# Kernel tuning notes

Hardware: AMD Instinct MI355X
Metric: run time of the kernel (lower is better)

## Reference

```python
import jax, jax.numpy as jnp
import numpy as np

B, S, E = 2, 2048, 1024
N_HEADS = 16
HEAD_DIM = E // N_HEADS  # 64
ATTN_SCALE = 1.0 / np.sqrt(E)  # NOTE: original scales by 1/sqrt(hidden_dim_phi), not head_dim
ROPE_BASE = 10000.0


def _rope(t):
    # t: (B, H, S, D) with D = HEAD_DIM; interleaved-pair RoPE (torchtune-style)
    d = t.shape[-1]
    s = t.shape[-2]
    inv_freq = 1.0 / (ROPE_BASE ** (jnp.arange(0, d, 2, dtype=jnp.float32) / d))  # (D/2,)
    ang = jnp.arange(s, dtype=jnp.float32)[:, None] * inv_freq[None, :]  # (S, D/2)
    cos, sin = jnp.cos(ang), jnp.sin(ang)  # (S, D/2)
    tp = t.reshape(t.shape[:-1] + (d // 2, 2))
    te, to = tp[..., 0], tp[..., 1]  # (B,H,S,D/2)
    oe = te * cos - to * sin
    oo = te * sin + to * cos
    return jnp.stack([oe, oo], axis=-1).reshape(t.shape)


def setup_inputs() -> dict:
    key = jax.random.key(0)
    ks = jax.random.split(key, 5)
    std = 0.02
    return {
        "x": jax.random.normal(ks[0], (B, S, E), dtype=jnp.float32),
        "W_q": jax.random.normal(ks[1], (E, E), dtype=jnp.float32) * std,
        "W_k": jax.random.normal(ks[2], (E, E), dtype=jnp.float32) * std,
        "W_v": jax.random.normal(ks[3], (E, E), dtype=jnp.float32) * std,
        "W_o": jax.random.normal(ks[4], (E, E), dtype=jnp.float32) * std,
    }


def reference(x, W_q, W_k, W_v, W_o):
    b, s, e = x.shape
    hd = e // N_HEADS
    # projections -> (B, H, S, D)
    def proj(w):
        return (x @ w).reshape(b, s, N_HEADS, hd).transpose(0, 2, 1, 3)
    q = _rope(proj(W_q))
    k = _rope(proj(W_k))
    v = proj(W_v)
    scores = jnp.einsum('bhsd,bhtd->bhst', q, k) * ATTN_SCALE  # (B,H,S,S)
    causal = jnp.triu(jnp.ones((s, s), dtype=bool), k=1)
    scores = jnp.where(causal, -jnp.inf, scores)
    probs = jax.nn.softmax(scores, axis=-1)  # dropout is identity in eval mode
    out = jnp.einsum('bhst,bhtd->bhsd', probs, v)
    out = out.transpose(0, 2, 1, 3).reshape(b, s, e)
    return out @ W_o
```

## Files before the change

kernel.cpp:

```cpp
#include <hip/hip_runtime.h>
#include <hip/hip_bf16.h>

#define S_LEN 2048
#define E_DIM 1024
#define NH 16
#define HD 64
#define ATTN_SCALE 0.03125f
#define QSCALE_L2E 0.045084312f
#define KVB 128

typedef __attribute__((ext_vector_type(8))) short short8;
typedef __attribute__((ext_vector_type(8))) unsigned short ushort8;
typedef __attribute__((ext_vector_type(4))) unsigned short ushort4_t;
typedef __attribute__((ext_vector_type(4))) float f32x4;
typedef __attribute__((ext_vector_type(4))) float f4;
typedef __attribute__((ext_vector_type(2))) unsigned int uint2_t;

__device__ __forceinline__ float bf2f(unsigned short u) {
    unsigned int x = ((unsigned int)u) << 16;
    return __builtin_bit_cast(float, x);
}
__device__ __forceinline__ unsigned short f2bf(float f) {
    unsigned int x = __builtin_bit_cast(unsigned int, f);
    x += 0x7FFFu + ((x >> 16) & 1u);
    return (unsigned short)(x >> 16);
}
__device__ __forceinline__ float exp2_fast(float x) {
    float r;
    asm("v_exp_f32 %0, %1" : "=v"(r) : "v"(x));
    return r;
}
__device__ __forceinline__ void gload16(const unsigned short* g, unsigned short* l) {
    __builtin_amdgcn_global_load_lds(
        (__attribute__((address_space(1))) void*)g,
        (__attribute__((address_space(3))) void*)l, 16, 0, 0);
}

__global__ __launch_bounds__(256) void k_prep(const float* __restrict__ x,
                                              unsigned short* __restrict__ xb,
                                              const float* W0, const float* W1,
                                              const float* W2, const float* W3,
                                              unsigned short* Tqkv,
                                              unsigned short* Twout,
                                              float* __restrict__ cosT,
                                              float* __restrict__ sinT) {
    int bid = blockIdx.x;
    int tid = threadIdx.x;
    if (bid < 2048) {
        size_t i = ((size_t)bid * 256 + tid) * 8;
        f4 a = *(const f4*)(x + i);
        f4 b = *(const f4*)(x + i + 4);
        ushort8 o;
        o[0] = f2bf(a[0]); o[1] = f2bf(a[1]); o[2] = f2bf(a[2]); o[3] = f2bf(a[3]);
        o[4] = f2bf(b[0]); o[5] = f2bf(b[1]); o[6] = f2bf(b[2]); o[7] = f2bf(b[3]);
        *(ushort8*)(xb + i) = o;
    } else if (bid < 2304) {
        int idx = (bid - 2048) * 256 + tid;
        int s = idx >> 5, j = idx & 31;
        float inv = expf(-(float)j * (9.210340371976184f / 32.f));
        float ang = (float)s * inv;
        cosT[idx] = cosf(ang);
        sinT[idx] = sinf(ang);
    } else {
        int t = bid - 2304;
        int bx = (t & 31) * 32, by = ((t >> 5) & 31) * 32, z = t >> 10;
        const float* W; unsigned short* T;
        switch (z) {
            case 0: W = W0; T = Tqkv; break;
            case 1: W = W1; T = Tqkv + 1048576; break;
            case 2: W = W2; T = Tqkv + 2097152; break;
            default: W = W3; T = Twout; break;
        }
        __shared__ float tile[32][33];
        int tx = tid & 31, ty = tid >> 5;
#pragma unroll
        for (int i = 0; i < 4; i++)
            tile[ty + i * 8][tx] = W[(size_t)(by + ty + i * 8) * E_DIM + bx + tx];
        __syncthreads();
#pragma unroll
        for (int i = 0; i < 4; i++)
            T[(size_t)(bx + ty + i * 8) * E_DIM + by + tx] = f2bf(tile[tx][ty + i * 8]);
    }
}

__global__ __launch_bounds__(256, 3)
void k_gemm97(const unsigned short* __restrict__ A,
              const unsigned short* __restrict__ B,
              unsigned short* __restrict__ Qo,
              unsigned short* __restrict__ Ko,
              unsigned short* __restrict__ Vto,
              const float* __restrict__ cosT,
              const float* __restrict__ sinT) {
    constexpr int NBN = 24;
    constexpr int NWG = 32 * NBN;
    __shared__ unsigned short Alds[128 * 64];
    __shared__ unsigned short Blds[128 * 64];
    int tid = threadIdx.x, lane = tid & 63, wid = tid >> 6;
    int l15 = lane & 15, lg = lane >> 4;
    int wr = wid >> 1, wc = wid & 1;
    int orig = blockIdx.y * NBN + blockIdx.x;
    int wg = (orig & 7) * (NWG / 8) + (orig >> 3);
    int bm = wg / NBN, bn = wg % NBN;

    f32x4 acc[4][4] = {};
    for (int k0 = 0; k0 < E_DIM; k0 += 64) {
#pragma unroll
        for (int i = 0; i < 4; i++) {
            int r = wid * 32 + i * 8 + (lane >> 3);
            int cs = (lane & 7) ^ (r & 7);
            gload16(A + (size_t)(bm * 128 + r) * E_DIM + k0 + cs * 8,
                    Alds + (wid * 256 + i * 64) * 8);
        }
#pragma unroll
        for (int i = 0; i < 4; i++) {
            int r = wid * 32 + i * 8 + (lane >> 3);
            int cs = (lane & 7) ^ (r & 7);
            gload16(B + (size_t)(bn * 128 + r) * E_DIM + k0 + cs * 8,
                    Blds + (wid * 256 + i * 64) * 8);
        }
        __syncthreads();
#pragma unroll
        for (int ks = 0; ks < 2; ks++) {
            short8 af[4], bfr[4];
#pragma unroll
            for (int mf = 0; mf < 4; mf++) {
                int r = wr * 64 + mf * 16 + l15;
                int gc = ks * 4 + lg;
                af[mf] = *(const short8*)(Alds + r * 64 + ((gc ^ (r & 7)) << 3));
            }
#pragma unroll
            for (int nf = 0; nf < 4; nf++) {
                int r = wc * 64 + nf * 16 + l15;
                int gc = ks * 4 + lg;
                bfr[nf] = *(const short8*)(Blds + r * 64 + ((gc ^ (r & 7)) << 3));
            }
            __builtin_amdgcn_s_setprio(1);
#pragma unroll
            for (int mf = 0; mf < 4; mf++)
#pragma unroll
                for (int nf = 0; nf < 4; nf++)
                    acc[mf][nf] = __builtin_amdgcn_mfma_f32_16x16x32_bf16(
                        af[mf], bfr[nf], acc[mf][nf], 0, 0, 0);
            __builtin_amdgcn_s_setprio(0);
        }
        __syncthreads();
    }
#pragma unroll
    for (int mf = 0; mf < 4; mf++) {
        int r0 = bm * 128 + wr * 64 + mf * 16 + lg * 4;
#pragma unroll
        for (int nf = 0; nf < 4; nf++) {
            int colg = bn * 128 + wc * 64 + nf * 16 + l15;
            int z = colg >> 10, c1 = colg & 1023;
            if (z == 2) {
                int h = c1 >> 6, d = c1 & 63;
                int bb = r0 >> 11, s = r0 & 2047;
                ushort4_t p;
#pragma unroll
                for (int r = 0; r < 4; r++) p[r] = f2bf(acc[mf][nf][r]);
                *(ushort4_t*)(Vto + (((size_t)((bb * 16 + h) * 64 + d)) << 11) + s) = p;
            } else {
                unsigned short* T = z ? Ko : Qo;
                int dl = c1 & 63, j = dl >> 1;
                float sgn = (dl & 1) ? 1.f : -1.f;
                float scq = z ? 1.f : QSCALE_L2E;
#pragma unroll
                for (int r = 0; r < 4; r++) {
                    int row = r0 + r, s = row & 2047;
                    float c = cosT[s * 32 + j], sn = sinT[s * 32 + j];
                    float v = acc[mf][nf][r];
                    float p = __shfl_xor(v, 1);
                    T[(size_t)row * E_DIM + c1] = f2bf((v * c + sgn * p * sn) * scq);
                }
            }
        }
    }
}

__global__ __launch_bounds__(256, 3)
void k_gemmo97(const unsigned short* __restrict__ A,
               const unsigned short* __restrict__ B,
               float* __restrict__ Fo) {
    constexpr int NBN = 16;
    constexpr int NWG = 32 * NBN;
    __shared__ unsigned short Alds[128 * 64];
    __shared__ unsigned short Blds[64 * 64];
    int tid = threadIdx.x, lane = tid & 63, wid = tid >> 6;
    int l15 = lane & 15, lg = lane >> 4;
    int wr = wid >> 1, wc = wid & 1;
    int orig = blockIdx.y * NBN + blockIdx.x;
    int wg = (orig & 7) * (NWG / 8) + (orig >> 3);
    int bm = wg / NBN, bn = wg % NBN;

    f32x4 acc[4][2] = {};
    for (int k0 = 0; k0 < E_DIM; k0 += 64) {
#pragma unroll
        for (int i = 0; i < 4; i++) {
            int r = wid * 32 + i * 8 + (lane >> 3);
            int cs = (lane & 7) ^ (r & 7);
            gload16(A + (size_t)(bm * 128 + r) * E_DIM + k0 + cs * 8,
                    Alds + (wid * 256 + i * 64) * 8);
        }
        {
#pragma unroll
            for (int i = 0; i < 2; i++) {
                int r = wid * 16 + i * 8 + (lane >> 3);
                int cs = (lane & 7) ^ (r & 7);
                gload16(B + (size_t)(bn * 64 + r) * E_DIM + k0 + cs * 8,
                        Blds + (wid * 128 + i * 64) * 8);
            }
        }
        __syncthreads();
#pragma unroll
        for (int ks = 0; ks < 2; ks++) {
            short8 af[4], bfr[2];
#pragma unroll
            for (int mf = 0; mf < 4; mf++) {
                int r = wr * 64 + mf * 16 + l15;
                int gc = ks * 4 + lg;
                af[mf] = *(const short8*)(Alds + r * 64 + ((gc ^ (r & 7)) << 3));
            }
#pragma unroll
            for (int nf = 0; nf < 2; nf++) {
                int r = wc * 32 + nf * 16 + l15;
                int gc = ks * 4 + lg;
                bfr[nf] = *(const short8*)(Blds + r * 64 + ((gc ^ (r & 7)) << 3));
            }
            __builtin_amdgcn_s_setprio(1);
#pragma unroll
            for (int mf = 0; mf < 4; mf++)
#pragma unroll
                for (int nf = 0; nf < 2; nf++)
                    acc[mf][nf] = __builtin_amdgcn_mfma_f32_16x16x32_bf16(
                        af[mf], bfr[nf], acc[mf][nf], 0, 0, 0);
            __builtin_amdgcn_s_setprio(0);
        }
        __syncthreads();
    }
#pragma unroll
    for (int mf = 0; mf < 4; mf++) {
        int r0 = bm * 128 + wr * 64 + mf * 16 + lg * 4;
#pragma unroll
        for (int nf = 0; nf < 2; nf++) {
            int colg = bn * 64 + wc * 32 + nf * 16 + l15;
#pragma unroll
            for (int r = 0; r < 4; r++)
                Fo[(size_t)(r0 + r) * E_DIM + colg] = acc[mf][nf][r];
        }
    }
}

__global__ __launch_bounds__(256, 3) void k_attn(const unsigned short* __restrict__ Q,
                                                 const unsigned short* __restrict__ K,
                                                 const unsigned short* __restrict__ Vt,
                                                 unsigned short* __restrict__ O) {
    __shared__ unsigned short K_lds[128 * 64];
    __shared__ unsigned short V_lds[64 * 128];
    __shared__ unsigned short P_lds[4][16][136];
    int tid = threadIdx.x, lane = tid & 63, wid = tid >> 6;
    int l15 = lane & 15, lg = lane >> 4;
    int orig = blockIdx.y * 32 + blockIdx.x;
    int xcd = orig & 7, idx = orig >> 3;
    int bh = xcd * 4 + (idx & 3);
    int qt = 31 - ((idx >> 2) & 31);
    int b = bh >> 4, h = bh & 15;
    const size_t base_qk = (size_t)b * S_LEN * E_DIM + (size_t)h * HD;
    const unsigned short* Vbh = Vt + ((size_t)(bh * 64) << 11);

    auto stageK = [&](int kt) {
        const unsigned short* Kb = K + base_qk + (size_t)(kt * KVB) * E_DIM;
#pragma unroll
        for (int i = 0; i < 4; i++) {
            int r = i * 32 + wid * 8 + (lane >> 3);
            int cs = (lane & 7) ^ (r & 7);
            gload16(Kb + (size_t)r * E_DIM + cs * 8, K_lds + i * 2048 + wid * 512);
        }
    };
    auto stageV = [&](int kt) {
#pragma unroll
        for (int i = 0; i < 4; i++) {
            int r = i * 16 + wid * 4 + (lane >> 4);
            int cs = (lane & 15) ^ (r & 7);
            gload16(Vbh + (size_t)r * 2048 + kt * KVB + cs * 8,
                    V_lds + i * 2048 + wid * 512);
        }
    };

    const unsigned short* Qb = Q + base_qk + (size_t)(qt * 64 + wid * 16) * E_DIM;
    short8 bq[2];
#pragma unroll
    for (int s2 = 0; s2 < 2; s2++)
        bq[s2] = *(const short8*)(Qb + (size_t)l15 * E_DIM + s2 * 32 + lg * 8);
    f32x4 acc_o[4] = {};
    float m_i = -1e30f, l_i = 0.f;
    int q_glob = qt * 64 + wid * 16 + l15;
    int nkt = (qt + 2) >> 1;
    stageK(0);
    stageV(0);
    asm volatile("s_waitcnt vmcnt(4)" ::: "memory");
    __builtin_amdgcn_s_barrier();
    __builtin_amdgcn_sched_barrier(0);
    for (int kt = 0; kt < nkt; ++kt) {
        f32x4 acc_s[8] = {};
        __builtin_amdgcn_s_setprio(1);
#pragma unroll
        for (int mf = 0; mf < 8; mf++) {
            int rK = mf * 16 + l15;
#pragma unroll
            for (int s2 = 0; s2 < 2; s2++) {
                int gc = s2 * 4 + lg;
                short8 a = *(const short8*)&K_lds[rK * 64 + ((gc ^ (rK & 7)) << 3)];
                acc_s[mf] = __builtin_amdgcn_mfma_f32_16x16x32_bf16(
                    a, bq[s2], acc_s[mf], 0, 0, 0);
            }
        }
        __builtin_amdgcn_s_setprio(0);
        __builtin_amdgcn_s_barrier();
        if (kt + 1 < nkt) stageK(kt + 1);
        float sv[32];
        float vmax = -1e30f;
        if (kt == nkt - 1) {
#pragma unroll
            for (int mf = 0; mf < 8; mf++)
#pragma unroll
                for (int r = 0; r < 4; r++) {
                    int kg = kt * KVB + mf * 16 + lg * 4 + r;
                    float v = acc_s[mf][r];
                    if (kg > q_glob) v = -1e30f;
                    sv[mf * 4 + r] = v;
                    vmax = fmaxf(vmax, v);
                }
        } else {
#pragma unroll
            for (int mf = 0; mf < 8; mf++)
#pragma unroll
                for (int r = 0; r < 4; r++) {
                    float v = acc_s[mf][r];
                    sv[mf * 4 + r] = v;
                    vmax = fmaxf(vmax, v);
                }
        }
        vmax = fmaxf(vmax, __shfl_xor(vmax, 16));
        vmax = fmaxf(vmax, __shfl_xor(vmax, 32));
        if (!__all(vmax - m_i <= 8.0f)) {
            float m_new = fmaxf(m_i, vmax);
            float corr = exp2_fast(m_i - m_new);
            l_i *= corr;
#pragma unroll
            for (int r = 0; r < 4; r++) {
                float c4 = __shfl(corr, lg * 4 + r);
#pragma unroll
                for (int nf = 0; nf < 4; nf++) acc_o[nf][r] *= c4;
            }
            m_i = m_new;
        }
        float rowsum = 0.f;
#pragma unroll
        for (int i = 0; i < 32; i++) {
            float p = exp2_fast(sv[i] - m_i);
            sv[i] = p;
            rowsum += p;
        }
        rowsum += __shfl_xor(rowsum, 16);
        rowsum += __shfl_xor(rowsum, 32);
        l_i += rowsum;
#pragma unroll
        for (int mf = 0; mf < 8; mf++) {
            unsigned int w0, w1;
            asm("v_cvt_pk_bf16_f32 %0, %1, %2"
                : "=v"(w0) : "v"(sv[mf * 4 + 0]), "v"(sv[mf * 4 + 1]));
            asm("v_cvt_pk_bf16_f32 %0, %1, %2"
                : "=v"(w1) : "v"(sv[mf * 4 + 2]), "v"(sv[mf * 4 + 3]));
            uint2_t w; w[0] = w0; w[1] = w1;
            *(uint2_t*)&P_lds[wid][l15][mf * 16 + lg * 4] = w;
        }
        if (kt + 1 < nkt)
            asm volatile("s_waitcnt vmcnt(4)" ::: "memory");
        else
            asm volatile("s_waitcnt vmcnt(0)" ::: "memory");
        __builtin_amdgcn_s_barrier();
        __builtin_amdgcn_sched_barrier(0);
        __builtin_amdgcn_s_setprio(1);
#pragma unroll
        for (int s2 = 0; s2 < 4; s2++) {
            short8 pa = *(const short8*)&P_lds[wid][l15][s2 * 32 + lg * 8];
#pragma unroll
            for (int nf = 0; nf < 4; nf++) {
                int rV = nf * 16 + l15;
                int gc = s2 * 4 + lg;
                short8 bv = *(const short8*)&V_lds[rV * 128 + ((gc ^ (rV & 7)) << 3)];
                acc_o[nf] = __builtin_amdgcn_mfma_f32_16x16x32_bf16(
                    pa, bv, acc_o[nf], 0, 0, 0);
            }
        }
        __builtin_amdgcn_s_setprio(0);
        __builtin_amdgcn_s_barrier();
        if (kt + 1 < nkt) {
            stageV(kt + 1);
            asm volatile("s_waitcnt vmcnt(4)" ::: "memory");
        }
        __builtin_amdgcn_s_barrier();
        __builtin_amdgcn_sched_barrier(0);
    }
    unsigned short* Ob = O + base_qk + (size_t)(qt * 64 + wid * 16) * E_DIM;
#pragma unroll
    for (int r = 0; r < 4; r++) {
        float linv = 1.f / __shfl(l_i, lg * 4 + r);
#pragma unroll
        for (int nf = 0; nf < 4; nf++)
            Ob[(size_t)(lg * 4 + r) * E_DIM + nf * 16 + l15] =
                f2bf(acc_o[nf][r] * linv);
    }
}

extern "C" void kernel_launch(void* const* d_in, const int* in_sizes, int n_in,
                              void* d_out, int out_size, void* d_ws, size_t ws_size,
                              hipStream_t stream) {
    (void)in_sizes; (void)n_in; (void)out_size; (void)ws_size;
    const float* x  = (const float*)d_in[0];
    const float* Wq = (const float*)d_in[1];
    const float* Wk = (const float*)d_in[2];
    const float* Wv = (const float*)d_in[3];
    const float* Wo = (const float*)d_in[4];

    unsigned short* us = (unsigned short*)d_ws;
    unsigned short* xb    = us;
    unsigned short* WqkvT = us + 4194304;
    unsigned short* WoT   = us + 7340032;
    unsigned short* Qb    = us + 8388608;
    unsigned short* Kb    = us + 12582912;
    unsigned short* Vt    = us + 16777216;
    unsigned short* AO    = us + 20971520;
    float* cosT = (float*)((char*)d_ws + 50331648);
    float* sinT = cosT + 65536;

    k_prep<<<6400, 256, 0, stream>>>(x, xb, Wq, Wk, Wv, Wo, WqkvT, WoT, cosT, sinT);
    k_gemm97<<<dim3(24, 32), 256, 0, stream>>>(xb, WqkvT, Qb, Kb, Vt, cosT, sinT);
    k_attn<<<dim3(32, 32), 256, 0, stream>>>(Qb, Kb, Vt, AO);
    k_gemmo97<<<dim3(16, 32), 256, 0, stream>>>(AO, WoT, (float*)d_out);
}
```

Baseline: 95.88 us.

## Rewrite attention with 32x32x16 MFMA, two waves per block, register-resident P

The attention kernel moves from 16x16x32 MFMAs with four waves of 16 query rows to 32x32x16 MFMAs with two waves of 32 query rows. The softmax probabilities now stay in registers, with a lane shuffle standing in for the P round trip through LDS. The lazy-rescale threshold is dropped in favour of an unconditional online-softmax correction. Output goes through an LDS staging buffer so each lane writes 16-byte vectors. This aims to cut LDS traffic and instruction count, but halving the threads per block means each wave issues twice as many K/V staging loads and there are fewer waves to hide latency.

```diff
diff --git a/kernel.cpp b/kernel.cpp
--- a/kernel.cpp
+++ b/kernel.cpp
@@ -13,8 +13,9 @@
 typedef __attribute__((ext_vector_type(8))) unsigned short ushort8;
 typedef __attribute__((ext_vector_type(4))) unsigned short ushort4_t;
 typedef __attribute__((ext_vector_type(4))) float f32x4;
+typedef __attribute__((ext_vector_type(16))) float f32x16;
 typedef __attribute__((ext_vector_type(4))) float f4;
-typedef __attribute__((ext_vector_type(2))) unsigned int uint2_t;
+typedef __attribute__((ext_vector_type(4))) unsigned int uint4v;
 
 __device__ __forceinline__ float bf2f(unsigned short u) {
     unsigned int x = ((unsigned int)u) << 16;
@@ -250,15 +251,15 @@
     }
 }
 
-__global__ __launch_bounds__(256, 3) void k_attn(const unsigned short* __restrict__ Q,
-                                                 const unsigned short* __restrict__ K,
-                                                 const unsigned short* __restrict__ Vt,
-                                                 unsigned short* __restrict__ O) {
+__global__ __launch_bounds__(128, 3)
+void k_attn(const unsigned short* __restrict__ Q,
+            const unsigned short* __restrict__ K,
+            const unsigned short* __restrict__ Vt,
+            unsigned short* __restrict__ O) {
     __shared__ unsigned short K_lds[128 * 64];
     __shared__ unsigned short V_lds[64 * 128];
-    __shared__ unsigned short P_lds[4][16][136];
     int tid = threadIdx.x, lane = tid & 63, wid = tid >> 6;
-    int l15 = lane & 15, lg = lane >> 4;
+    int l31 = lane & 31, hi = lane >> 5;
     int orig = blockIdx.y * 32 + blockIdx.x;
     int xcd = orig & 7, idx = orig >> 3;
     int bh = xcd * 4 + (idx & 3);
@@ -267,149 +268,166 @@
     const size_t base_qk = (size_t)b * S_LEN * E_DIM + (size_t)h * HD;
     const unsigned short* Vbh = Vt + ((size_t)(bh * 64) << 11);
 
+    int qbase = qt * 64 + wid * 32;
+    int q_glob = qbase + l31;
+    int nkt = (qt + 2) >> 1;
+    int swz = l31 & 7;
+    bool ishi = hi != 0;
+
     auto stageK = [&](int kt) {
         const unsigned short* Kb = K + base_qk + (size_t)(kt * KVB) * E_DIM;
 #pragma unroll
-        for (int i = 0; i < 4; i++) {
-            int r = i * 32 + wid * 8 + (lane >> 3);
+        for (int i = 0; i < 8; i++) {
+            int r = i * 16 + wid * 8 + (lane >> 3);
             int cs = (lane & 7) ^ (r & 7);
-            gload16(Kb + (size_t)r * E_DIM + cs * 8, K_lds + i * 2048 + wid * 512);
+            gload16(Kb + (size_t)r * E_DIM + cs * 8,
+                    K_lds + i * 1024 + wid * 512 + 0);
         }
     };
     auto stageV = [&](int kt) {
 #pragma unroll
-        for (int i = 0; i < 4; i++) {
-            int r = i * 16 + wid * 4 + (lane >> 4);
-            int cs = (lane & 15) ^ (r & 7);
+        for (int i = 0; i < 8; i++) {
+            int r = i * 8 + wid * 4 + (lane >> 4);
+            int c = lane & 15;
+            int cs = c ^ (r & 7);
             gload16(Vbh + (size_t)r * 2048 + kt * KVB + cs * 8,
-                    V_lds + i * 2048 + wid * 512);
+                    V_lds + i * 1024 + wid * 512);
         }
     };
 
-    const unsigned short* Qb = Q + base_qk + (size_t)(qt * 64 + wid * 16) * E_DIM;
-    short8 bq[2];
-#pragma unroll
-    for (int s2 = 0; s2 < 2; s2++)
-        bq[s2] = *(const short8*)(Qb + (size_t)l15 * E_DIM + s2 * 32 + lg * 8);
-    f32x4 acc_o[4] = {};
+    const unsigned short* Qb = Q + base_qk + (size_t)(wid * 32 + l31) * E_DIM
+                                 - (size_t)(wid * 32 + l31) * E_DIM
+                                 + (size_t)q_glob * E_DIM;
+    short8 qf[4];
+#pragma unroll
+    for (int s = 0; s < 4; s++)
+        qf[s] = *(const short8*)(Qb + s * 16 + hi * 8);
+
+    f32x16 ot0 = {}, ot1 = {};
     float m_i = -1e30f, l_i = 0.f;
-    int q_glob = qt * 64 + wid * 16 + l15;
-    int nkt = (qt + 2) >> 1;
+
     stageK(0);
     stageV(0);
-    asm volatile("s_waitcnt vmcnt(4)" ::: "memory");
+    asm volatile("s_waitcnt vmcnt(8)" ::: "memory");
     __builtin_amdgcn_s_barrier();
     __builtin_amdgcn_sched_barrier(0);
     for (int kt = 0; kt < nkt; ++kt) {
-        f32x4 acc_s[8] = {};
+        f32x16 st[4] = {};
         __builtin_amdgcn_s_setprio(1);
 #pragma unroll
-        for (int mf = 0; mf < 8; mf++) {
-            int rK = mf * 16 + l15;
-#pragma unroll
-            for (int s2 = 0; s2 < 2; s2++) {
-                int gc = s2 * 4 + lg;
-                short8 a = *(const short8*)&K_lds[rK * 64 + ((gc ^ (rK & 7)) << 3)];
-                acc_s[mf] = __builtin_amdgcn_mfma_f32_16x16x32_bf16(
-                    a, bq[s2], acc_s[mf], 0, 0, 0);
+        for (int g = 0; g < 4; g++) {
+            int row = g * 32 + l31;
+#pragma unroll
+            for (int s = 0; s < 4; s++) {
+                short8 ka = *(const short8*)
+                    &K_lds[row * 64 + (((s * 2 + hi) ^ swz) << 3)];
+                st[g] = __builtin_amdgcn_mfma_f32_32x32x16_bf16(ka, qf[s], st[g], 0, 0, 0);
             }
         }
         __builtin_amdgcn_s_setprio(0);
         __builtin_amdgcn_s_barrier();
         if (kt + 1 < nkt) stageK(kt + 1);
-        float sv[32];
         float vmax = -1e30f;
-        if (kt == nkt - 1) {
-#pragma unroll
-            for (int mf = 0; mf < 8; mf++)
-#pragma unroll
-                for (int r = 0; r < 4; r++) {
-                    int kg = kt * KVB + mf * 16 + lg * 4 + r;
-                    float v = acc_s[mf][r];
-                    if (kg > q_glob) v = -1e30f;
-                    sv[mf * 4 + r] = v;
+        bool domask = (kt * KVB + 127) > qbase;
+        if (domask) {
+#pragma unroll
+            for (int g = 0; g < 4; g++)
+#pragma unroll
+                for (int r = 0; r < 16; r++) {
+                    int kg = kt * KVB + g * 32 + (r & 3) + 8 * (r >> 2) + 4 * hi;
+                    float v = (kg > q_glob) ? -1e30f : st[g][r];
+                    st[g][r] = v;
                     vmax = fmaxf(vmax, v);
                 }
         } else {
 #pragma unroll
-            for (int mf = 0; mf < 8; mf++)
-#pragma unroll
-                for (int r = 0; r < 4; r++) {
-                    float v = acc_s[mf][r];
-                    sv[mf * 4 + r] = v;
-                    vmax = fmaxf(vmax, v);
-                }
-        }
-        vmax = fmaxf(vmax, __shfl_xor(vmax, 16));
+            for (int g = 0; g < 4; g++)
+#pragma unroll
+                for (int r = 0; r < 16; r++)
+                    vmax = fmaxf(vmax, st[g][r]);
+        }
         vmax = fmaxf(vmax, __shfl_xor(vmax, 32));
-        if (!__all(vmax - m_i <= 8.0f)) {
-            float m_new = fmaxf(m_i, vmax);
-            float corr = exp2_fast(m_i - m_new);
-            l_i *= corr;
-#pragma unroll
-            for (int r = 0; r < 4; r++) {
-                float c4 = __shfl(corr, lg * 4 + r);
-#pragma unroll
-                for (int nf = 0; nf < 4; nf++) acc_o[nf][r] *= c4;
-            }
-            m_i = m_new;
-        }
-        float rowsum = 0.f;
-#pragma unroll
-        for (int i = 0; i < 32; i++) {
-            float p = exp2_fast(sv[i] - m_i);
-            sv[i] = p;
-            rowsum += p;
-        }
-        rowsum += __shfl_xor(rowsum, 16);
-        rowsum += __shfl_xor(rowsum, 32);
-        l_i += rowsum;
-#pragma unroll
-        for (int mf = 0; mf < 8; mf++) {
-            unsigned int w0, w1;
-            asm("v_cvt_pk_bf16_f32 %0, %1, %2"
-                : "=v"(w0) : "v"(sv[mf * 4 + 0]), "v"(sv[mf * 4 + 1]));
-            asm("v_cvt_pk_bf16_f32 %0, %1, %2"
-                : "=v"(w1) : "v"(sv[mf * 4 + 2]), "v"(sv[mf * 4 + 3]));
-            uint2_t w; w[0] = w0; w[1] = w1;
-            *(uint2_t*)&P_lds[wid][l15][mf * 16 + lg * 4] = w;
-        }
+        float m_new = fmaxf(m_i, vmax);
+        float corr = exp2_fast(m_i - m_new);
+        float rs = 0.f;
+#pragma unroll
+        for (int g = 0; g < 4; g++)
+#pragma unroll
+            for (int r = 0; r < 16; r++) {
+                float p = exp2_fast(st[g][r] - m_new);
+                st[g][r] = p;
+                rs += p;
+            }
+        rs += __shfl_xor(rs, 32);
+        l_i = l_i * corr + rs;
+        m_i = m_new;
+        unsigned int pk[4][8];
+#pragma unroll
+        for (int g = 0; g < 4; g++)
+#pragma unroll
+            for (int i = 0; i < 8; i++)
+                asm("v_cvt_pk_bf16_f32 %0, %1, %2"
+                    : "=v"(pk[g][i]) : "v"(st[g][2 * i]), "v"(st[g][2 * i + 1]));
         if (kt + 1 < nkt)
-            asm volatile("s_waitcnt vmcnt(4)" ::: "memory");
+            asm volatile("s_waitcnt vmcnt(8)" ::: "memory");
         else
             asm volatile("s_waitcnt vmcnt(0)" ::: "memory");
         __builtin_amdgcn_s_barrier();
         __builtin_amdgcn_sched_barrier(0);
+#pragma unroll
+        for (int r = 0; r < 16; r++) { ot0[r] *= corr; ot1[r] *= corr; }
         __builtin_amdgcn_s_setprio(1);
 #pragma unroll
-        for (int s2 = 0; s2 < 4; s2++) {
-            short8 pa = *(const short8*)&P_lds[wid][l15][s2 * 32 + lg * 8];
-#pragma unroll
-            for (int nf = 0; nf < 4; nf++) {
-                int rV = nf * 16 + l15;
-                int gc = s2 * 4 + lg;
-                short8 bv = *(const short8*)&V_lds[rV * 128 + ((gc ^ (rV & 7)) << 3)];
-                acc_o[nf] = __builtin_amdgcn_mfma_f32_16x16x32_bf16(
-                    pa, bv, acc_o[nf], 0, 0, 0);
-            }
-        }
+        for (int g = 0; g < 4; g++)
+#pragma unroll
+            for (int ks = 0; ks < 2; ks++) {
+                int off = ks * 4;
+                unsigned int a  = pk[g][off + 0], b2 = pk[g][off + 1];
+                unsigned int c2 = pk[g][off + 2], d2 = pk[g][off + 3];
+                unsigned int sa = __shfl_xor(a, 32),  sb = __shfl_xor(b2, 32);
+                unsigned int sc = __shfl_xor(c2, 32), sd = __shfl_xor(d2, 32);
+                uint4v w;
+                w[0] = ishi ? sc : a;  w[1] = ishi ? sd : b2;
+                w[2] = ishi ? c2 : sa; w[3] = ishi ? d2 : sb;
+                short8 pf = __builtin_bit_cast(short8, w);
+                int gc = g * 4 + ks * 2 + hi;
+                short8 va0 = *(const short8*)
+                    &V_lds[l31 * 128 + ((gc ^ swz) << 3)];
+                short8 va1 = *(const short8*)
+                    &V_lds[(32 + l31) * 128 + ((gc ^ swz) << 3)];
+                ot0 = __builtin_amdgcn_mfma_f32_32x32x16_bf16(va0, pf, ot0, 0, 0, 0);
+                ot1 = __builtin_amdgcn_mfma_f32_32x32x16_bf16(va1, pf, ot1, 0, 0, 0);
+            }
         __builtin_amdgcn_s_setprio(0);
         __builtin_amdgcn_s_barrier();
         if (kt + 1 < nkt) {
             stageV(kt + 1);
-            asm volatile("s_waitcnt vmcnt(4)" ::: "memory");
-        }
-        __builtin_amdgcn_s_barrier();
-        __builtin_amdgcn_sched_barrier(0);
-    }
-    unsigned short* Ob = O + base_qk + (size_t)(qt * 64 + wid * 16) * E_DIM;
-#pragma unroll
-    for (int r = 0; r < 4; r++) {
-        float linv = 1.f / __shfl(l_i, lg * 4 + r);
-#pragma unroll
-        for (int nf = 0; nf < 4; nf++)
-            Ob[(size_t)(lg * 4 + r) * E_DIM + nf * 16 + l15] =
-                f2bf(acc_o[nf][r] * linv);
+            asm volatile("s_waitcnt vmcnt(8)" ::: "memory");
+            __builtin_amdgcn_s_barrier();
+            __builtin_amdgcn_sched_barrier(0);
+        }
+    }
+    float linv = 1.f / l_i;
+    unsigned short* scb = K_lds + wid * 2304;
+#pragma unroll
+    for (int i = 0; i < 8; i++) {
+        int d = 2 * (i & 1) + 8 * (i >> 1) + 4 * hi;
+        unsigned int w0, w1;
+        float a0 = ot0[2 * i] * linv, a1 = ot0[2 * i + 1] * linv;
+        float b0 = ot1[2 * i] * linv, b1 = ot1[2 * i + 1] * linv;
+        asm("v_cvt_pk_bf16_f32 %0, %1, %2" : "=v"(w0) : "v"(a0), "v"(a1));
+        asm("v_cvt_pk_bf16_f32 %0, %1, %2" : "=v"(w1) : "v"(b0), "v"(b1));
+        *(unsigned int*)&scb[l31 * 72 + d] = w0;
+        *(unsigned int*)&scb[l31 * 72 + 32 + d] = w1;
+    }
+    asm volatile("s_waitcnt lgkmcnt(0)" ::: "memory");
+    __builtin_amdgcn_sched_barrier(0);
+    int qr = lane >> 1, half = (lane & 1) * 32;
+    unsigned short* Ob = O + base_qk + (size_t)(qbase + qr) * E_DIM;
+#pragma unroll
+    for (int j = 0; j < 4; j++) {
+        short8 vv = *(const short8*)&scb[qr * 72 + half + j * 8];
+        *(short8*)(Ob + half + j * 8) = vv;
     }
 }
 
@@ -436,6 +454,6 @@
 
     k_prep<<<6400, 256, 0, stream>>>(x, xb, Wq, Wk, Wv, Wo, WqkvT, WoT, cosT, sinT);
     k_gemm97<<<dim3(24, 32), 256, 0, stream>>>(xb, WqkvT, Qb, Kb, Vt, cosT, sinT);
-    k_attn<<<dim3(32, 32), 256, 0, stream>>>(Qb, Kb, Vt, AO);
+    k_attn<<<dim3(32, 32), 128, 0, stream>>>(Qb, Kb, Vt, AO);
     k_gemmo97<<<dim3(16, 32), 256, 0, stream>>>(AO, WoT, (float*)d_out);
 }
```

Measured after the change: 177.5 us. 1.85x slower.
